# Optimization experiments

Measured on AMD Instinct MI355X. Metric: run time of the kernel, lower is better.

## Reference

```python
import jax, jax.numpy as jnp
import numpy as np

# Neuron hyperparameters (mid-range of the optuna search space)
THRESHOLD = 1.0
CURRENT_DECAY = 0.3
VOLTAGE_DECAY = 0.8
TAU_GRAD = 0.5
SCALE_GRAD = 1.0

B, N_IN, H, N_OUT, T = 64, 2048, 1024, 2, 128
SPIKE_RATE = 0.1  # input spike density


@jax.custom_vjp
def spike_fn(v):
    # Heaviside spike with SLAYER exponential surrogate gradient
    return (v >= 0.0).astype(v.dtype)

def _spike_fwd(v):
    return spike_fn(v), v

def _spike_bwd(v, g):
    return (g * SCALE_GRAD * jnp.exp(-jnp.abs(v) / TAU_GRAD),)

spike_fn.defvjp(_spike_fwd, _spike_bwd)


def cuba_dense(spike, W):
    """One SLAYER CUBA Dense block: dense synapse + leaky IF neuron over time.
    spike: [B, N_in, T], W: [N_out, N_in] -> [B, N_out, T] output spikes."""
    z = jnp.einsum('oi,bit->tbo', W, spike)  # synaptic current input, [T, B, O]
    O = W.shape[0]
    zeros = jnp.zeros((spike.shape[0], O), spike.dtype)

    def step(carry, z_t):
        cur, vol = carry
        cur = cur * (1.0 - CURRENT_DECAY) + z_t          # current dynamics
        vol = vol * (1.0 - VOLTAGE_DECAY) + cur          # voltage dynamics
        s = spike_fn(vol - THRESHOLD)                    # threshold spike
        vol = vol * (1.0 - s)                            # reset to zero on spike
        return (cur, vol), s

    _, s = jax.lax.scan(step, (zeros, zeros), z)
    return jnp.transpose(s, (1, 2, 0))  # [B, O, T]


def setup_inputs() -> dict:
    key = jax.random.key(0)
    k0, k1, k2, k3 = jax.random.split(key, 4)
    spike = (jax.random.uniform(k0, (B, N_IN, T)) < SPIKE_RATE).astype(jnp.float32)
    W1 = jax.random.normal(k1, (H, N_IN), jnp.float32) / np.sqrt(N_IN).astype(np.float32)
    W2 = jax.random.normal(k2, (H, H), jnp.float32) / np.sqrt(H).astype(np.float32)
    W3 = jax.random.normal(k3, (N_OUT, H), jnp.float32) / np.sqrt(H).astype(np.float32)
    return {"spike": spike, "W1": W1, "W2": W2, "W3": W3}


def reference(spike, W1, W2, W3):
    s = cuba_dense(spike, W1)
    s = cuba_dense(s, W2)
    s = cuba_dense(s, W3)
    return s  # [B, 2, T]
```

## Files before the change

### kernel.cpp

```cpp
#include <hip/hip_runtime.h>


typedef unsigned short ushort_t;
typedef unsigned int uint_t;
typedef unsigned char uchar_t;
typedef int i32x4 __attribute__((ext_vector_type(4)));

#define S1F 0.00390625f
#define S2F 3.0517578125e-5f
#define S3F 2.384185791015625e-7f

__device__ __forceinline__ void glds16(const uchar_t* g, uchar_t* l) {
  __builtin_amdgcn_global_load_lds(
      (const __attribute__((address_space(1))) uint_t*)g,
      (__attribute__((address_space(3))) uint_t*)l, 16, 0, 0);
}

__global__ __launch_bounds__(256) void prep(const float* __restrict__ W1,
                                            const float* __restrict__ W2,
                                            const float* __restrict__ spike,
                                            char* __restrict__ w1q1,
                                            char* __restrict__ w1q2,
                                            char* __restrict__ w1q3,
                                            char* __restrict__ w2q1,
                                            char* __restrict__ w2q2,
                                            char* __restrict__ w2q3,
                                            uchar_t* __restrict__ A1) {
  const int tid = threadIdx.x;
  if (blockIdx.x < 3072) {
    const float* W;
    char *p1, *p2, *p3;
    size_t e0;
    if (blockIdx.x < 2048) {
      W = W1; p1 = w1q1; p2 = w1q2; p3 = w1q3;
      e0 = (size_t)blockIdx.x * 1024 + tid * 4;
    } else {
      W = W2; p1 = w2q1; p2 = w2q2; p3 = w2q3;
      e0 = (size_t)(blockIdx.x - 2048) * 1024 + tid * 4;
    }
    float4 w = *(const float4*)(W + e0);
    char4 c1, c2, c3;
    float q, r;
#define QUANT(comp, f1, f2, f3)                    \
    q = rintf((comp) * 256.0f);  f1 = (char)(int)q; \
    r = (comp) - q * S1F;                           \
    q = rintf(r * 32768.0f);     f2 = (char)(int)q; \
    r = r - q * S2F;                                \
    q = rintf(r * 4194304.0f);   f3 = (char)(int)q;
    QUANT(w.x, c1.x, c2.x, c3.x)
    QUANT(w.y, c1.y, c2.y, c3.y)
    QUANT(w.z, c1.z, c2.z, c3.z)
    QUANT(w.w, c1.w, c2.w, c3.w)
#undef QUANT
    *(char4*)(p1 + e0) = c1;
    *(char4*)(p2 + e0) = c2;
    *(char4*)(p3 + e0) = c3;
    return;
  }
  __shared__ uchar_t lds8[128 * 132];
  const int bid = blockIdx.x - 3072;
  const int b = bid >> 4;
  const int i0 = (bid & 15) * 128;
#pragma unroll
  for (int it = 0; it < 16; ++it) {
    int p = it * 256 + tid;
    int i = p >> 5, tg = (p & 31) * 4;
    float4 v = *(const float4*)(spike + ((size_t)b * 2048 + i0 + i) * 128 + tg);
    uint_t pk = (v.x != 0.0f ? 1u : 0u) | (v.y != 0.0f ? 1u : 0u) << 8 |
                (v.z != 0.0f ? 1u : 0u) << 16 | (v.w != 0.0f ? 1u : 0u) << 24;
    *(uint_t*)(lds8 + i * 132 + tg) = pk;
  }
  __syncthreads();
#pragma unroll
  for (int it = 0; it < 16; ++it) {
    int p = it * 256 + tid;
    int t = p >> 5, jw = p & 31;
    uint_t u = (uint_t)lds8[(4 * jw + 0) * 132 + t] |
               ((uint_t)lds8[(4 * jw + 1) * 132 + t] << 8) |
               ((uint_t)lds8[(4 * jw + 2) * 132 + t] << 16) |
               ((uint_t)lds8[(4 * jw + 3) * 132 + t] << 24);
    *(uint_t*)(A1 + (size_t)(b * 128 + t) * 2048 + i0 + jw * 4) = u;
  }
}

__global__ __launch_bounds__(256, 4)
void gemm_scan(const uchar_t* __restrict__ A, const char* __restrict__ Q1,
               const char* __restrict__ Q2, const char* __restrict__ Q3,
               uchar_t* __restrict__ S, int K) {
  __shared__ float smemf[7168];
  uchar_t* sA = (uchar_t*)smemf;
  float* Zt = smemf;

  const int tid = threadIdx.x;
  const int wave = tid >> 6, lane = tid & 63;
  const int m0 = blockIdx.y * 128;
  const int o0 = blockIdx.x * 32;
  const int qm = wave >> 1, qn = wave & 1;
  const int fr = lane & 15, q = lane >> 4;

  i32x4 acc[4][3];
#pragma unroll
  for (int i = 0; i < 4; ++i)
#pragma unroll
    for (int p = 0; p < 3; ++p) acc[i][p] = (i32x4){0, 0, 0, 0};

  const char* qplanes[3] = {Q1, Q2, Q3};
  const uchar_t* gsrc[7];
  uchar_t* ldst[7];
#pragma unroll
  for (int it = 0; it < 7; ++it) {
    int s = it * 256 + tid;
    ldst[it] = sA + (size_t)(it * 256 + wave * 64) * 16;
    if (s < 1024) {
      int row = s >> 3;
      int u0 = (s & 7) ^ (row & 7);
      gsrc[it] = A + (size_t)(m0 + row) * K + u0 * 16;
    } else {
      int t2 = s - 1024;
      int p = t2 >> 8, r = (t2 >> 3) & 31;
      int u0 = (t2 & 7) ^ (r & 7);
      gsrc[it] = (const uchar_t*)qplanes[p] + (size_t)(o0 + r) * K + u0 * 16;
    }
  }

  int aoff[4][2], boff[3][2];
#pragma unroll
  for (int i = 0; i < 4; ++i) {
    int row = qm * 64 + i * 16 + fr;
#pragma unroll
    for (int hh = 0; hh < 2; ++hh)
      aoff[i][hh] = (row * 8 + ((hh * 4 + q) ^ (row & 7))) * 16;
  }
  {
    int row = qn * 16 + fr;
#pragma unroll
    for (int hh = 0; hh < 2; ++hh) {
      int phys = row * 8 + ((hh * 4 + q) ^ (row & 7));
#pragma unroll
      for (int p = 0; p < 3; ++p)
        boff[p][hh] = (1024 + p * 256 + phys) * 16;
    }
  }

  for (int kc = 0; kc < K; kc += 128) {
#pragma unroll
    for (int it = 0; it < 7; ++it) glds16(gsrc[it] + kc, ldst[it]);
    __syncthreads();

#pragma unroll
    for (int hh = 0; hh < 2; ++hh) {
      i32x4 af[4], bq[3];
#pragma unroll
      for (int i = 0; i < 4; ++i) af[i] = *(const i32x4*)(sA + aoff[i][hh]);
#pragma unroll
      for (int p = 0; p < 3; ++p) bq[p] = *(const i32x4*)(sA + boff[p][hh]);
#pragma unroll
      for (int p = 0; p < 3; ++p)
#pragma unroll
        for (int i = 0; i < 4; ++i)
          acc[i][p] = __builtin_amdgcn_mfma_i32_16x16x64_i8(af[i], bq[p], acc[i][p], 0, 0, 0);
    }
    __syncthreads();
  }

#pragma unroll
  for (int i = 0; i < 4; ++i)
#pragma unroll
    for (int rr = 0; rr < 4; ++rr) {
      int t = qm * 64 + i * 16 + q * 4 + rr;
      float z = (float)acc[i][0][rr] * S1F + (float)acc[i][1][rr] * S2F +
                (float)acc[i][2][rr] * S3F;
      Zt[t * 33 + qn * 16 + fr] = z;
    }
  __syncthreads();

  if (tid < 32) {
#pragma clang fp contract(off)
    float cur = 0.0f, vol = 0.0f;
    const int o = o0 + tid;
    for (int t = 0; t < 128; ++t) {
      float z = Zt[t * 33 + tid];
      cur = cur * 0.7f;
      cur = cur + z;
      vol = vol * 0.2f;
      vol = vol + cur;
      float v = vol - 1.0f;
      float s = (v >= 0.0f) ? 1.0f : 0.0f;
      vol = vol * (1.0f - s);
      S[(size_t)(m0 + t) * 1024 + o] = (v >= 0.0f) ? 1u : 0u;
    }
  }
}

__global__ __launch_bounds__(256) void gemm3_scan(const uchar_t* __restrict__ X,
                                                  const float* __restrict__ W3,
                                                  float* __restrict__ out) {
  __shared__ float w3s[2048];
  __shared__ float z3[256];
  __shared__ float sp[256];
  const int tid = threadIdx.x;
  const int b = blockIdx.x;
  for (int i = tid; i < 2048; i += 256) w3s[i] = W3[i];
  __syncthreads();
  const int wave = tid >> 6, lane = tid & 63;
  for (int tt = 0; tt < 32; ++tt) {
    int t = wave * 32 + tt;
    const uint4* rp = (const uint4*)(X + (size_t)(b * 128 + t) * 1024);
    uint4 v = rp[lane];
    float s0 = 0.0f, s1 = 0.0f;
    const uint_t uw[4] = {v.x, v.y, v.z, v.w};
#pragma unroll
    for (int wq = 0; wq < 4; ++wq)
#pragma unroll
      for (int c = 0; c < 4; ++c) {
        float x = (float)((uw[wq] >> (8 * c)) & 1u);
        int i0 = lane * 16 + wq * 4 + c;
        s0 = fmaf(x, w3s[i0], s0);
        s1 = fmaf(x, w3s[1024 + i0], s1);
      }
#pragma unroll
    for (int off = 32; off > 0; off >>= 1) {
      s0 += __shfl_down(s0, off);
      s1 += __shfl_down(s1, off);
    }
    if (lane == 0) {
      z3[t * 2] = s0;
      z3[t * 2 + 1] = s1;
    }
  }
  __syncthreads();
  if (tid < 2) {
#pragma clang fp contract(off)
    float cur = 0.0f, vol = 0.0f;
    for (int t = 0; t < 128; ++t) {
      float z = z3[t * 2 + tid];
      cur = cur * 0.7f;
      cur = cur + z;
      vol = vol * 0.2f;
      vol = vol + cur;
      float v = vol - 1.0f;
      float s = (v >= 0.0f) ? 1.0f : 0.0f;
      vol = vol * (1.0f - s);
      sp[tid * 128 + t] = s;
    }
  }
  __syncthreads();
  out[b * 256 + tid] = sp[tid];
}

extern "C" void kernel_launch(void* const* d_in, const int* in_sizes, int n_in,
                              void* d_out, int out_size, void* d_ws, size_t ws_size,
                              hipStream_t stream) {
  const float* spike = (const float*)d_in[0];
  const float* W1 = (const float*)d_in[1];
  const float* W2 = (const float*)d_in[2];
  const float* W3 = (const float*)d_in[3];
  float* out = (float*)d_out;

  char* ws = (char*)d_ws;
  const size_t MB = 1024 * 1024;
  uchar_t* A1 = (uchar_t*)ws;
  uchar_t* S2 = (uchar_t*)(ws + 16 * MB);
  uchar_t* S3 = (uchar_t*)(ws + 24 * MB);
  char* w1q1 = ws + 32 * MB;
  char* w1q2 = ws + 34 * MB;
  char* w1q3 = ws + 36 * MB;
  char* w2q1 = ws + 38 * MB;
  char* w2q2 = ws + 39 * MB;
  char* w2q3 = ws + 40 * MB;

  prep<<<4096, 256, 0, stream>>>(W1, W2, spike, w1q1, w1q2, w1q3, w2q1, w2q2,
                                 w2q3, A1);
  gemm_scan<<<dim3(32, 64), 256, 0, stream>>>(A1, w1q1, w1q2, w1q3, S2, 2048);
  gemm_scan<<<dim3(32, 64), 256, 0, stream>>>(S2, w2q1, w2q2, w2q3, S3, 1024);
  gemm3_scan<<<64, 256, 0, stream>>>(S3, W3, out);
}
```

Before: 220.1 us.

## Widen gemm_scan output tile from 32 to 64 neurons per block

Each block now computes 64 output neurons instead of 32, giving each wave two 16-column B fragments and 24 accumulators. Every A fragment loaded from LDS is reused across twice as many MFMAs, and the A tile is fetched from global memory half as often. The grid shrinks to 16x64 blocks, and 64 threads now run the neuron scan instead of 32. The trade-off is more LDS (40KB) and more accumulator registers, which may lower occupancy, plus fewer blocks to spread across CUs.

```diff
diff --git a/kernel.cpp b/kernel.cpp
--- a/kernel.cpp
+++ b/kernel.cpp
@@ -87,28 +87,30 @@
 void gemm_scan(const uchar_t* __restrict__ A, const char* __restrict__ Q1,
                const char* __restrict__ Q2, const char* __restrict__ Q3,
                uchar_t* __restrict__ S, int K) {
-  __shared__ float smemf[7168];
+  __shared__ float smemf[10240];
   uchar_t* sA = (uchar_t*)smemf;
   float* Zt = smemf;
 
   const int tid = threadIdx.x;
   const int wave = tid >> 6, lane = tid & 63;
   const int m0 = blockIdx.y * 128;
-  const int o0 = blockIdx.x * 32;
+  const int o0 = blockIdx.x * 64;
   const int qm = wave >> 1, qn = wave & 1;
   const int fr = lane & 15, q = lane >> 4;
 
-  i32x4 acc[4][3];
+  i32x4 acc[4][2][3];
 #pragma unroll
   for (int i = 0; i < 4; ++i)
 #pragma unroll
-    for (int p = 0; p < 3; ++p) acc[i][p] = (i32x4){0, 0, 0, 0};
+    for (int j = 0; j < 2; ++j)
+#pragma unroll
+      for (int p = 0; p < 3; ++p) acc[i][j][p] = (i32x4){0, 0, 0, 0};
 
   const char* qplanes[3] = {Q1, Q2, Q3};
-  const uchar_t* gsrc[7];
-  uchar_t* ldst[7];
-#pragma unroll
-  for (int it = 0; it < 7; ++it) {
+  const uchar_t* gsrc[10];
+  uchar_t* ldst[10];
+#pragma unroll
+  for (int it = 0; it < 10; ++it) {
     int s = it * 256 + tid;
     ldst[it] = sA + (size_t)(it * 256 + wave * 64) * 16;
     if (s < 1024) {
@@ -117,13 +119,14 @@
       gsrc[it] = A + (size_t)(m0 + row) * K + u0 * 16;
     } else {
       int t2 = s - 1024;
-      int p = t2 >> 8, r = (t2 >> 3) & 31;
-      int u0 = (t2 & 7) ^ (r & 7);
-      gsrc[it] = (const uchar_t*)qplanes[p] + (size_t)(o0 + r) * K + u0 * 16;
-    }
-  }
-
-  int aoff[4][2], boff[3][2];
+      int p = t2 >> 9, w = t2 & 511;
+      int row = w >> 3;
+      int u0 = (w & 7) ^ (row & 7);
+      gsrc[it] = (const uchar_t*)qplanes[p] + (size_t)(o0 + row) * K + u0 * 16;
+    }
+  }
+
+  int aoff[4][2], boff[3][2][2];
 #pragma unroll
   for (int i = 0; i < 4; ++i) {
     int row = qm * 64 + i * 16 + fr;
@@ -131,34 +134,39 @@
     for (int hh = 0; hh < 2; ++hh)
       aoff[i][hh] = (row * 8 + ((hh * 4 + q) ^ (row & 7))) * 16;
   }
-  {
-    int row = qn * 16 + fr;
+#pragma unroll
+  for (int j = 0; j < 2; ++j) {
+    int row = qn * 32 + j * 16 + fr;
 #pragma unroll
     for (int hh = 0; hh < 2; ++hh) {
-      int phys = row * 8 + ((hh * 4 + q) ^ (row & 7));
+      int rel = row * 8 + ((hh * 4 + q) ^ (row & 7));
 #pragma unroll
       for (int p = 0; p < 3; ++p)
-        boff[p][hh] = (1024 + p * 256 + phys) * 16;
+        boff[p][j][hh] = (1024 + p * 512 + rel) * 16;
     }
   }
 
   for (int kc = 0; kc < K; kc += 128) {
 #pragma unroll
-    for (int it = 0; it < 7; ++it) glds16(gsrc[it] + kc, ldst[it]);
+    for (int it = 0; it < 10; ++it) glds16(gsrc[it] + kc, ldst[it]);
     __syncthreads();
 
 #pragma unroll
     for (int hh = 0; hh < 2; ++hh) {
-      i32x4 af[4], bq[3];
+      i32x4 af[4], bq[3][2];
 #pragma unroll
       for (int i = 0; i < 4; ++i) af[i] = *(const i32x4*)(sA + aoff[i][hh]);
 #pragma unroll
-      for (int p = 0; p < 3; ++p) bq[p] = *(const i32x4*)(sA + boff[p][hh]);
-#pragma unroll
       for (int p = 0; p < 3; ++p)
 #pragma unroll
+        for (int j = 0; j < 2; ++j) bq[p][j] = *(const i32x4*)(sA + boff[p][j][hh]);
+#pragma unroll
+      for (int p = 0; p < 3; ++p)
+#pragma unroll
         for (int i = 0; i < 4; ++i)
-          acc[i][p] = __builtin_amdgcn_mfma_i32_16x16x64_i8(af[i], bq[p], acc[i][p], 0, 0, 0);
+#pragma unroll
+          for (int j = 0; j < 2; ++j)
+            acc[i][j][p] = __builtin_amdgcn_mfma_i32_16x16x64_i8(af[i], bq[p][j], acc[i][j][p], 0, 0, 0);
     }
     __syncthreads();
   }
@@ -166,20 +174,22 @@
 #pragma unroll
   for (int i = 0; i < 4; ++i)
 #pragma unroll
-    for (int rr = 0; rr < 4; ++rr) {
-      int t = qm * 64 + i * 16 + q * 4 + rr;
-      float z = (float)acc[i][0][rr] * S1F + (float)acc[i][1][rr] * S2F +
-                (float)acc[i][2][rr] * S3F;
-      Zt[t * 33 + qn * 16 + fr] = z;
-    }
-  __syncthreads();
-
-  if (tid < 32) {
+    for (int j = 0; j < 2; ++j)
+#pragma unroll
+      for (int rr = 0; rr < 4; ++rr) {
+        int t = qm * 64 + i * 16 + q * 4 + rr;
+        float z = (float)acc[i][j][0][rr] * S1F + (float)acc[i][j][1][rr] * S2F +
+                  (float)acc[i][j][2][rr] * S3F;
+        Zt[t * 65 + qn * 32 + j * 16 + fr] = z;
+      }
+  __syncthreads();
+
+  if (tid < 64) {
 #pragma clang fp contract(off)
     float cur = 0.0f, vol = 0.0f;
     const int o = o0 + tid;
     for (int t = 0; t < 128; ++t) {
-      float z = Zt[t * 33 + tid];
+      float z = Zt[t * 65 + tid];
       cur = cur * 0.7f;
       cur = cur + z;
       vol = vol * 0.2f;
@@ -271,7 +281,7 @@
 
   prep<<<4096, 256, 0, stream>>>(W1, W2, spike, w1q1, w1q2, w1q3, w2q1, w2q2,
                                  w2q3, A1);
-  gemm_scan<<<dim3(32, 64), 256, 0, stream>>>(A1, w1q1, w1q2, w1q3, S2, 2048);
-  gemm_scan<<<dim3(32, 64), 256, 0, stream>>>(S2, w2q1, w2q2, w2q3, S3, 1024);
+  gemm_scan<<<dim3(16, 64), 256, 0, stream>>>(A1, w1q1, w1q2, w1q3, S2, 2048);
+  gemm_scan<<<dim3(16, 64), 256, 0, stream>>>(S2, w2q1, w2q2, w2q3, S3, 1024);
   gemm3_scan<<<64, 256, 0, stream>>>(S3, W3, out);
 }
```

After: 266.4 us. 1.21x slower.
